# Performance work log

Measured on AMD Instinct MI355X. Metric: run time of the kernel, lower is better.

The kernel has to match this reference:

```python
import jax, jax.numpy as jnp
import numpy as np
from jax import lax

B, D, N, M = 512, 1024, 8192, 2048  # batch, input_dim, n_sdr, n_minicolumns
K = 4            # n_columns
W_SPARSE = 320   # SDR sparsity w (active bits per SDR)
K_ACTIVE = 40    # active minicolumns per step
PERM_THRESH = 0.5
LR = 0.01
CONSENSUS_THRESH = 1.0  # strict AND


def setup_inputs() -> dict:
    key = jax.random.key(0)
    k1, k2, k3 = jax.random.split(key, 3)
    s_batch = jax.random.normal(k1, (B, D), dtype=jnp.float32)
    W_enc = jax.random.normal(k2, (K, D, N), dtype=jnp.float32)  # per-column encoders (no weight sharing)
    perm = jax.random.uniform(k3, (K, M, N), dtype=jnp.float32)  # per-column permanences
    return {"s_batch": s_batch, "W_enc": W_enc, "perm": perm}


def _one_hot_topk(scores, k):
    # scores: [B, C] -> binary [B, C] with top-k per row set to 1
    _, idx = lax.top_k(scores, k)
    rows = jnp.arange(scores.shape[0])[:, None]
    return jnp.zeros_like(scores).at[rows, idx].set(1.0)


def reference(s_batch, W_enc, perm):
    def column(We, P):
        # SDRSpace.encode: random projection + top-w binarization
        scores = s_batch @ We                       # [B, N]
        sdr = _one_hot_topk(scores, W_SPARSE)       # [B, N] binary
        # SpatialPooler.forward_batch: overlap with connected synapses, top-k minicolumns
        connected = (P >= PERM_THRESH).astype(sdr.dtype)  # [M, N]
        overlap = sdr @ connected.T                 # [B, M]
        act = _one_hot_topk(overlap, K_ACTIVE)      # [B, M] binary winners
        # hebbian_update_batch: reinforce active inputs, punish inactive, on winning columns
        delta = (LR / B) * (act.T @ (2.0 * sdr - 1.0))    # [M, N] scatter-accumulated
        P_new = jnp.clip(P + delta, 0.0, 1.0)
        return sdr, P_new

    all_sdrs, perms_new = jax.vmap(column)(W_enc, perm)   # [K,B,N], [K,M,N]
    vote_fraction = all_sdrs.mean(axis=0)                  # [B, N]
    consensus = (vote_fraction >= CONSENSUS_THRESH).astype(jnp.float32)
    return consensus, all_sdrs[0], perms_new
```

## Files before the change

kernel.cpp:

```cpp
#include <hip/hip_runtime.h>
#include <stdint.h>

#define B_   512
#define D_   1024
#define N_   8192
#define M_   2048
#define K_   4
#define WSP  320
#define KACT 40
#define NW   128

typedef _Float16 f16;
typedef _Float16 f16x4 __attribute__((ext_vector_type(4)));
typedef _Float16 f16x8 __attribute__((ext_vector_type(8)));
typedef float f32x4 __attribute__((ext_vector_type(4)));

#define BM 128
#define BN 256
#define SPLIT_SCALE 2048.0f
#define SPLIT_INV (1.0f / 2048.0f)

#define GLD16(g, l) __builtin_amdgcn_global_load_lds( \
    (const __attribute__((address_space(1))) uint32_t*)(g), \
    (__attribute__((address_space(3))) uint32_t*)(l), 16, 0, 0)

__global__ __launch_bounds__(256) void prep_kernel(const float* __restrict__ perm,
                                                   uint32_t* __restrict__ conn32,
                                                   int* __restrict__ mcount,
                                                   const float* __restrict__ S,
                                                   uint8_t* __restrict__ imgA) {
    int bid = blockIdx.x;
    int tid = threadIdx.x;
    if (bid < 128) {
        int blk = bid;
        int mt = blk >> 5, dstep = blk & 31;
        uint8_t* outb = imgA + (size_t)blk * 16384;
#pragma unroll
        for (int q = 0; q < 4; q++) {
            int o = tid * 16 + q * 4096;
            int r = o >> 7, inner = o & 127;
            int sw = (r & 7) << 4;
            int raw = inner ^ sw;
            int plane = raw >> 6;
            int k0 = (raw & 63) >> 1;
            const float* sp = &S[(size_t)(mt * 128 + r) * D_ + dstep * 32 + k0];
            float4 v0 = *(const float4*)sp;
            float4 v1 = *(const float4*)(sp + 4);
            f16x8 out;
            if (plane == 0) {
                out[0] = (f16)v0.x; out[1] = (f16)v0.y; out[2] = (f16)v0.z; out[3] = (f16)v0.w;
                out[4] = (f16)v1.x; out[5] = (f16)v1.y; out[6] = (f16)v1.z; out[7] = (f16)v1.w;
            } else {
                f16 h0 = (f16)v0.x, h1 = (f16)v0.y, h2 = (f16)v0.z, h3 = (f16)v0.w;
                f16 h4 = (f16)v1.x, h5 = (f16)v1.y, h6 = (f16)v1.z, h7 = (f16)v1.w;
                out[0] = (f16)((v0.x - (float)h0) * SPLIT_SCALE);
                out[1] = (f16)((v0.y - (float)h1) * SPLIT_SCALE);
                out[2] = (f16)((v0.z - (float)h2) * SPLIT_SCALE);
                out[3] = (f16)((v0.w - (float)h3) * SPLIT_SCALE);
                out[4] = (f16)((v1.x - (float)h4) * SPLIT_SCALE);
                out[5] = (f16)((v1.y - (float)h5) * SPLIT_SCALE);
                out[6] = (f16)((v1.z - (float)h6) * SPLIT_SCALE);
                out[7] = (f16)((v1.w - (float)h7) * SPLIT_SCALE);
            }
            *(f16x8*)&outb[o] = out;
        }
        return;
    }
    int km = bid - 128;
    if (tid == 0) mcount[km] = 0;
    const float* p = perm + (size_t)km * N_ + tid * 32;
    uint32_t bits = 0;
#pragma unroll
    for (int q = 0; q < 8; q++) {
        float4 v = *(const float4*)&p[q * 4];
        bits |= (v.x >= 0.5f ? 1u : 0u) << (q * 4 + 0);
        bits |= (v.y >= 0.5f ? 1u : 0u) << (q * 4 + 1);
        bits |= (v.z >= 0.5f ? 1u : 0u) << (q * 4 + 2);
        bits |= (v.w >= 0.5f ? 1u : 0u) << (q * 4 + 3);
    }
    conn32[(size_t)km * 256 + tid] = bits;
}

__device__ __forceinline__ void pack_write_B(uint8_t* Bn, const float* w,
                                             int kc0, int bn, int bsw) {
#pragma unroll
    for (int kci = 0; kci < 2; kci++) {
        int kc = kc0 * 2 + kci;
        f16x8 hv, lv;
#pragma unroll
        for (int j = 0; j < 8; j++) {
            float x = w[kci * 8 + j];
            f16 h = (f16)x;
            hv[j] = h;
            lv[j] = (f16)((x - (float)h) * SPLIT_SCALE);
        }
        *(f16x8*)&Bn[bn * 128 + ((kc * 16) ^ bsw)] = hv;
        *(f16x8*)&Bn[bn * 128 + ((64 + kc * 16) ^ bsw)] = lv;
    }
}

__global__ __launch_bounds__(512, 2) void gemm_kernel(const uint8_t* __restrict__ imgA,
                                                      const float* __restrict__ W,
                                                      float* __restrict__ C) {
    __shared__ __align__(16) uint8_t lds[98304];

    int bid = blockIdx.x;
    int l = (bid & 7) * 64 + (bid >> 3);
    int mt = l & 3, nt = (l >> 2) & 31, kt = l >> 7;

    int tid = threadIdx.x;
    int wave = tid >> 6, lane = tid & 63;
    int wm = wave >> 2, wn = wave & 3;
    int lr = lane & 15, lg = lane >> 4;

    const uint8_t* srcA0 = imgA + (size_t)(mt * 32) * 16384 + wave * 1024 + lane * 16;

    const float* Wp = W + (size_t)kt * D_ * N_ + nt * BN;
    float* Cp = C + (size_t)kt * B_ * N_ + (size_t)(mt * BM) * N_ + nt * BN;

    int bn = tid & 255;
    int kc0 = tid >> 8;
    int bsw = (bn & 7) << 4;

    f32x4 acc0[4][4], acc1[4][4];
#pragma unroll
    for (int i = 0; i < 4; i++)
#pragma unroll
        for (int j = 0; j < 4; j++) {
            acc0[i][j] = (f32x4){0.f, 0.f, 0.f, 0.f};
            acc1[i][j] = (f32x4){0.f, 0.f, 0.f, 0.f};
        }

    {
        uint8_t* dA = lds + wave * 1024;
        GLD16(srcA0, dA);
        GLD16(srcA0 + 8192, dA + 8192);
        float w[16];
        const float* wp0 = Wp + (size_t)(kc0 * 16) * N_ + bn;
#pragma unroll
        for (int j = 0; j < 16; j++) w[j] = wp0[(size_t)j * N_];
        pack_write_B(lds + 32768, w, kc0, bn, bsw);
    }
    __syncthreads();

    for (int dstep = 0; dstep < 32; dstep++) {
        int cur = dstep & 1;
        uint8_t* Ac = lds + cur * 16384;
        uint8_t* Bc = lds + 32768 + cur * 32768;
        bool pf = (dstep < 31);

        float wreg[16];
        if (pf) {
            const uint8_t* sA = srcA0 + (size_t)(dstep + 1) * 16384;
            uint8_t* dA = lds + (cur ^ 1) * 16384 + wave * 1024;
            GLD16(sA, dA);
            GLD16(sA + 8192, dA + 8192);
            const float* wp0 = Wp + (size_t)((dstep + 1) * 32 + kc0 * 16) * N_ + bn;
#pragma unroll
            for (int j = 0; j < 16; j++) wreg[j] = wp0[(size_t)j * N_];
        }

        f16x8 ah[4], al[4];
#pragma unroll
        for (int i = 0; i < 4; i++) {
            int r = wm * 64 + i * 16 + lr;
            int sw = (r & 7) << 4;
            ah[i] = *(const f16x8*)&Ac[r * 128 + ((lg * 16) ^ sw)];
            al[i] = *(const f16x8*)&Ac[r * 128 + ((64 + lg * 16) ^ sw)];
        }
#pragma unroll
        for (int jj = 0; jj < 4; jj++) {
            int n = wn * 64 + jj * 16 + lr;
            int sw = (n & 7) << 4;
            f16x8 bh = *(const f16x8*)&Bc[n * 128 + ((lg * 16) ^ sw)];
            f16x8 bl = *(const f16x8*)&Bc[n * 128 + ((64 + lg * 16) ^ sw)];
            __builtin_amdgcn_s_setprio(1);
#pragma unroll
            for (int i = 0; i < 4; i++) {
                acc0[i][jj] = __builtin_amdgcn_mfma_f32_16x16x32_f16(ah[i], bh, acc0[i][jj], 0, 0, 0);
                acc1[i][jj] = __builtin_amdgcn_mfma_f32_16x16x32_f16(ah[i], bl, acc1[i][jj], 0, 0, 0);
                acc1[i][jj] = __builtin_amdgcn_mfma_f32_16x16x32_f16(al[i], bh, acc1[i][jj], 0, 0, 0);
            }
            __builtin_amdgcn_s_setprio(0);
        }

        if (pf)
            pack_write_B(lds + 32768 + (cur ^ 1) * 32768, wreg, kc0, bn, bsw);

        __syncthreads();
    }

#pragma unroll
    for (int i = 0; i < 4; i++)
#pragma unroll
        for (int jj = 0; jj < 4; jj++) {
            int r0 = wm * 64 + i * 16 + lg * 4;
            int c0 = wn * 64 + jj * 16 + lr;
#pragma unroll
            for (int r = 0; r < 4; r++)
                Cp[(size_t)(r0 + r) * N_ + c0] = acc0[i][jj][r] + acc1[i][jj][r] * SPLIT_INV;
        }
}

__global__ __launch_bounds__(256) void sdr_select_kernel(const float* __restrict__ scores,
                                                         uint32_t* __restrict__ sdr_bits32) {
    __shared__ int hist[256];
    __shared__ int scan2[256];
    __shared__ uint32_t sh_prefix;
    __shared__ int sh_r;

    int b = blockIdx.x;
    int k = blockIdx.y;
    int tid = threadIdx.x;
    const float* row = scores + ((size_t)k * B_ + b) * N_ + tid * 32;

    uint32_t key[32];
#pragma unroll
    for (int q = 0; q < 8; q++) {
        float4 v = *(const float4*)&row[q * 4];
        uint32_t u0 = __float_as_uint(v.x), u1 = __float_as_uint(v.y);
        uint32_t u2 = __float_as_uint(v.z), u3 = __float_as_uint(v.w);
        key[q * 4 + 0] = (u0 & 0x80000000u) ? ~u0 : (u0 | 0x80000000u);
        key[q * 4 + 1] = (u1 & 0x80000000u) ? ~u1 : (u1 | 0x80000000u);
        key[q * 4 + 2] = (u2 & 0x80000000u) ? ~u2 : (u2 | 0x80000000u);
        key[q * 4 + 3] = (u3 & 0x80000000u) ? ~u3 : (u3 | 0x80000000u);
    }
    if (tid == 0) { sh_prefix = 0u; sh_r = WSP; }
    __syncthreads();

    for (int p = 3; p >= 0; p--) {
        hist[tid] = 0;
        __syncthreads();
        uint32_t prefix = sh_prefix;
        int r = sh_r;
        uint32_t maskHi = (p == 3) ? 0u : (0xFFFFFFFFu << ((p + 1) * 8));
        int shift = p * 8;
#pragma unroll
        for (int j = 0; j < 32; j++) {
            uint32_t u = key[j];
            if ((u & maskHi) == prefix) atomicAdd(&hist[(u >> shift) & 255], 1);
        }
        __syncthreads();
#pragma unroll
        for (int off = 1; off < 256; off <<= 1) {
            int x = hist[tid] + ((tid + off < 256) ? hist[tid + off] : 0);
            __syncthreads();
            hist[tid] = x;
            __syncthreads();
        }
        int Sv = hist[tid];
        int Sn = (tid < 255) ? hist[tid + 1] : 0;
        if (Sv >= r && Sn < r) { sh_prefix = prefix | ((uint32_t)tid << shift); sh_r = r - Sn; }
        __syncthreads();
    }
    uint32_t t = sh_prefix;

    int gt = 0, eq = 0;
#pragma unroll
    for (int j = 0; j < 32; j++) {
        gt += (key[j] > t); eq += (key[j] == t);
    }
    hist[tid] = gt; scan2[tid] = eq;
    __syncthreads();
#pragma unroll
    for (int off = 1; off < 256; off <<= 1) {
        int g = hist[tid] + ((tid >= off) ? hist[tid - off] : 0);
        int e = scan2[tid] + ((tid >= off) ? scan2[tid - off] : 0);
        __syncthreads();
        hist[tid] = g; scan2[tid] = e;
        __syncthreads();
    }
    int totalGt = hist[255];
    int eb = scan2[tid] - eq;
    int r_eq = WSP - totalGt;

    uint32_t bits = 0;
#pragma unroll
    for (int j = 0; j < 32; j++) {
        uint32_t u = key[j];
        bool f = (u > t) || ((u == t) && (eb < r_eq));
        if (u == t) eb++;
        if (f) bits |= (1u << j);
    }
    sdr_bits32[((size_t)k * B_ + b) * 256 + tid] = bits;
}

#define OV_BBLK 16
#define OV_MTILE 512
__global__ __launch_bounds__(256) void overlap_mat_kernel(const uint64_t* __restrict__ sdr_bits,
                                                          const uint64_t* __restrict__ conn,
                                                          uint16_t* __restrict__ ovmat) {
    __shared__ uint64_t sw[OV_BBLK][NW];

    int bid = blockIdx.x;
    int nb = (bid & 7) * 64 + (bid >> 3);
    int k = nb >> 7;
    int rem = nb & 127;
    int b0 = (rem >> 2) * OV_BBLK;
    int m0 = (rem & 3) * OV_MTILE;
    int tid = threadIdx.x;

    for (int i = tid; i < OV_BBLK * NW; i += 256) {
        int bb = i >> 7, w = i & 127;
        sw[bb][w] = sdr_bits[((size_t)k * B_ + b0 + bb) * NW + w];
    }
    __syncthreads();

    int m_a = m0 + tid;
    int m_b = m0 + tid + 256;
    const ulonglong2* cra = (const ulonglong2*)(conn + ((size_t)k * M_ + m_a) * NW);
    const ulonglong2* crb = (const ulonglong2*)(conn + ((size_t)k * M_ + m_b) * NW);

    int acca[OV_BBLK], accb[OV_BBLK];
#pragma unroll
    for (int i = 0; i < OV_BBLK; i++) { acca[i] = 0; accb[i] = 0; }

#pragma unroll 2
    for (int wp = 0; wp < NW / 2; wp++) {
        ulonglong2 ca = cra[wp];
        ulonglong2 cb = crb[wp];
#pragma unroll
        for (int bb = 0; bb < OV_BBLK; bb++) {
            ulonglong2 s = *(const ulonglong2*)&sw[bb][wp * 2];
            acca[bb] += __popcll(ca.x & s.x) + __popcll(ca.y & s.y);
            accb[bb] += __popcll(cb.x & s.x) + __popcll(cb.y & s.y);
        }
    }
#pragma unroll
    for (int bb = 0; bb < OV_BBLK; bb++) {
        ovmat[((size_t)k * B_ + b0 + bb) * M_ + m_a] = (uint16_t)acca[bb];
        ovmat[((size_t)k * B_ + b0 + bb) * M_ + m_b] = (uint16_t)accb[bb];
    }
}

__global__ __launch_bounds__(256) void top40_kernel(const uint16_t* __restrict__ ovmat,
                                                    int* __restrict__ mcount,
                                                    int* __restrict__ mlist) {
    __shared__ int hist[512];
    __shared__ int scanbuf[256];
    __shared__ int sh_t, sh_req;

    int kb = blockIdx.x;
    int k = kb >> 9;
    int b = kb & 511;
    int tid = threadIdx.x;

    union { uint4 raw; uint16_t v[8]; } ov;
    ov.raw = *(const uint4*)&ovmat[(size_t)kb * M_ + tid * 8];

    hist[tid] = 0; hist[tid + 256] = 0;
    __syncthreads();
#pragma unroll
    for (int j = 0; j < 8; j++) atomicAdd(&hist[ov.v[j]], 1);
    __syncthreads();
#pragma unroll
    for (int off = 1; off < 512; off <<= 1) {
        int a0 = hist[tid] + ((tid + off < 512) ? hist[tid + off] : 0);
        int a1 = hist[tid + 256] + ((tid + 256 + off < 512) ? hist[tid + 256 + off] : 0);
        __syncthreads();
        hist[tid] = a0; hist[tid + 256] = a1;
        __syncthreads();
    }
#pragma unroll
    for (int which = 0; which < 2; which++) {
        int v = tid + which * 256;
        int Sv = hist[v];
        int Sn = (v < 511) ? hist[v + 1] : 0;
        if (Sv >= KACT && Sn < KACT) { sh_t = v; sh_req = KACT - Sn; }
    }
    __syncthreads();
    int t = sh_t, req = sh_req;
    int eq = 0;
#pragma unroll
    for (int j = 0; j < 8; j++) eq += (ov.v[j] == t);
    scanbuf[tid] = eq;
    __syncthreads();
#pragma unroll
    for (int off = 1; off < 256; off <<= 1) {
        int e = scanbuf[tid] + ((tid >= off) ? scanbuf[tid - off] : 0);
        __syncthreads();
        scanbuf[tid] = e;
        __syncthreads();
    }
    int eb = scanbuf[tid] - eq;
#pragma unroll
    for (int j = 0; j < 8; j++) {
        int m = tid * 8 + j;
        int v2 = ov.v[j];
        bool act = (v2 > t) || (v2 == t && eb < req);
        if (v2 == t) eb++;
        if (act) {
            int pos = atomicAdd(&mcount[k * M_ + m], 1);
            mlist[(((size_t)k * M_ + m) << 9) + pos] = b;
        }
    }
}

__global__ __launch_bounds__(512) void tail_kernel(const float* __restrict__ perm,
                                                   const uint64_t* __restrict__ sdr_bits,
                                                   const int* __restrict__ mcount,
                                                   const int* __restrict__ mlist,
                                                   float* __restrict__ pout,
                                                   float* __restrict__ cons,
                                                   float* __restrict__ sdr0) {
    __shared__ int blist[512];
    if (blockIdx.x >= 8192) {
        int gid = (blockIdx.x - 8192) * 512 + threadIdx.x;
        int b = gid >> 13;
        int n = gid & (N_ - 1);
        int wi = n >> 6, bit = n & 63;
        size_t base = (size_t)b * NW + wi;
        uint64_t w0 = sdr_bits[base];
        uint64_t w1 = sdr_bits[(size_t)1 * B_ * NW + base];
        uint64_t w2 = sdr_bits[(size_t)2 * B_ * NW + base];
        uint64_t w3 = sdr_bits[(size_t)3 * B_ * NW + base];
        uint64_t a = w0 & w1 & w2 & w3;
        cons[gid] = (float)((a >> bit) & 1);
        sdr0[gid] = (float)((w0 >> bit) & 1);
        return;
    }
    int km = blockIdx.x;
    int k = km / M_;
    int tid = threadIdx.x;
    int cnt = mcount[km];
    for (int i = tid; i < cnt; i += 512) blist[i] = mlist[((size_t)km << 9) + i];
    __syncthreads();

    int n0 = tid * 16;
    int c[16];
#pragma unroll
    for (int j = 0; j < 16; j++) c[j] = 0;
    int wi = n0 >> 6;
    int sh = n0 & 63;
    const uint64_t* sb = sdr_bits + (size_t)k * B_ * NW;
    for (int i = 0; i < cnt; i++) {
        uint64_t wv = sb[(size_t)blist[i] * NW + wi];
        unsigned bits = (unsigned)((wv >> sh) & 0xFFFFu);
#pragma unroll
        for (int j = 0; j < 16; j++) c[j] += (bits >> j) & 1;
    }
    const float scale = (float)(0.01 / 512.0);
    const float* pr = perm + (size_t)km * N_ + n0;
    float* po = pout + (size_t)km * N_ + n0;
#pragma unroll
    for (int q = 0; q < 4; q++) {
        float4 pv = *(const float4*)&pr[q * 4];
        float4 o;
        o.x = fminf(fmaxf(pv.x + scale * (float)(2 * c[q * 4 + 0] - cnt), 0.f), 1.f);
        o.y = fminf(fmaxf(pv.y + scale * (float)(2 * c[q * 4 + 1] - cnt), 0.f), 1.f);
        o.z = fminf(fmaxf(pv.z + scale * (float)(2 * c[q * 4 + 2] - cnt), 0.f), 1.f);
        o.w = fminf(fmaxf(pv.w + scale * (float)(2 * c[q * 4 + 3] - cnt), 0.f), 1.f);
        *(float4*)&po[q * 4] = o;
    }
}

extern "C" void kernel_launch(void* const* d_in, const int* in_sizes, int n_in,
                              void* d_out, int out_size, void* d_ws, size_t ws_size,
                              hipStream_t stream) {
    const float* s_batch = (const float*)d_in[0];
    const float* W_enc   = (const float*)d_in[1];
    const float* perm    = (const float*)d_in[2];

    float* out  = (float*)d_out;
    float* cons = out;
    float* sdr0 = out + (size_t)B_ * N_;
    float* pout = out + (size_t)2 * B_ * N_;

    char* ws = (char*)d_ws;
    float*    scores   = (float*)ws;
    uint16_t* ovmat    = (uint16_t*)ws;
    uint64_t* sdr_bits = (uint64_t*)(ws + ((size_t)64 << 20));
    uint64_t* conn     = (uint64_t*)(ws + ((size_t)66 << 20));
    int*      mcount   = (int*)(ws + ((size_t)74 << 20));
    int*      mlist    = (int*)(ws + ((size_t)75 << 20));
    uint8_t*  imgA     = (uint8_t*)(ws + ((size_t)92 << 20));

    prep_kernel<<<8192 + 128, 256, 0, stream>>>(perm, (uint32_t*)conn, mcount,
                                                s_batch, imgA);

    gemm_kernel<<<K_ * (B_ / BM) * (N_ / BN), 512, 0, stream>>>(imgA, W_enc, scores);

    dim3 gs(B_, K_);
    sdr_select_kernel<<<gs, 256, 0, stream>>>(scores, (uint32_t*)sdr_bits);

    overlap_mat_kernel<<<K_ * (B_ / OV_BBLK) * (M_ / OV_MTILE), 256, 0, stream>>>(
        sdr_bits, conn, ovmat);
    top40_kernel<<<K_ * B_, 256, 0, stream>>>(ovmat, mcount, mlist);

    tail_kernel<<<16384, 512, 0, stream>>>(perm, sdr_bits, mcount, mlist,
                                           pout, cons, sdr0);
}
```

Before: 450.5 us.

## Switch top-k selection kernels to one row per wavefront with shuffle scans

The SDR top-320 and overlap top-40 selection kernels now handle one row per 64-lane wavefront instead of one row per 256-thread block. Block-wide shared-memory scans with many __syncthreads are replaced by wave shuffles and ballots. The SDR radix select drops from four 8-bit passes to three 11/11/10-bit passes over a per-wave 2048-bin histogram. Rows are re-read from global memory on each pass instead of kept in registers, trading extra (likely cached) loads for fewer barriers and fewer passes.

```diff
diff --git a/kernel.cpp b/kernel.cpp
--- a/kernel.cpp
+++ b/kernel.cpp
@@ -23,6 +23,10 @@
 #define GLD16(g, l) __builtin_amdgcn_global_load_lds( \
     (const __attribute__((address_space(1))) uint32_t*)(g), \
     (__attribute__((address_space(3))) uint32_t*)(l), 16, 0, 0)
+
+__device__ __forceinline__ uint32_t fkey(uint32_t u) {
+    return u ^ ((uint32_t)((int32_t)u >> 31) | 0x80000000u);
+}
 
 __global__ __launch_bounds__(256) void prep_kernel(const float* __restrict__ perm,
                                                    uint32_t* __restrict__ conn32,
@@ -204,85 +208,111 @@
 
 __global__ __launch_bounds__(256) void sdr_select_kernel(const float* __restrict__ scores,
                                                          uint32_t* __restrict__ sdr_bits32) {
-    __shared__ int hist[256];
-    __shared__ int scan2[256];
-    __shared__ uint32_t sh_prefix;
-    __shared__ int sh_r;
-
-    int b = blockIdx.x;
-    int k = blockIdx.y;
+    __shared__ uint32_t hist4[4][2048];
     int tid = threadIdx.x;
-    const float* row = scores + ((size_t)k * B_ + b) * N_ + tid * 32;
-
-    uint32_t key[32];
-#pragma unroll
-    for (int q = 0; q < 8; q++) {
-        float4 v = *(const float4*)&row[q * 4];
-        uint32_t u0 = __float_as_uint(v.x), u1 = __float_as_uint(v.y);
-        uint32_t u2 = __float_as_uint(v.z), u3 = __float_as_uint(v.w);
-        key[q * 4 + 0] = (u0 & 0x80000000u) ? ~u0 : (u0 | 0x80000000u);
-        key[q * 4 + 1] = (u1 & 0x80000000u) ? ~u1 : (u1 | 0x80000000u);
-        key[q * 4 + 2] = (u2 & 0x80000000u) ? ~u2 : (u2 | 0x80000000u);
-        key[q * 4 + 3] = (u3 & 0x80000000u) ? ~u3 : (u3 | 0x80000000u);
-    }
-    if (tid == 0) { sh_prefix = 0u; sh_r = WSP; }
-    __syncthreads();
-
-    for (int p = 3; p >= 0; p--) {
-        hist[tid] = 0;
-        __syncthreads();
-        uint32_t prefix = sh_prefix;
-        int r = sh_r;
-        uint32_t maskHi = (p == 3) ? 0u : (0xFFFFFFFFu << ((p + 1) * 8));
-        int shift = p * 8;
-#pragma unroll
-        for (int j = 0; j < 32; j++) {
-            uint32_t u = key[j];
-            if ((u & maskHi) == prefix) atomicAdd(&hist[(u >> shift) & 255], 1);
-        }
-        __syncthreads();
-#pragma unroll
-        for (int off = 1; off < 256; off <<= 1) {
-            int x = hist[tid] + ((tid + off < 256) ? hist[tid + off] : 0);
-            __syncthreads();
-            hist[tid] = x;
-            __syncthreads();
-        }
-        int Sv = hist[tid];
-        int Sn = (tid < 255) ? hist[tid + 1] : 0;
-        if (Sv >= r && Sn < r) { sh_prefix = prefix | ((uint32_t)tid << shift); sh_r = r - Sn; }
-        __syncthreads();
-    }
-    uint32_t t = sh_prefix;
+    int w = tid >> 6, lane = tid & 63;
+    int r = blockIdx.x * 4 + w;
+    uint32_t* hist = hist4[w];
+    const float* rowp = scores + (size_t)r * N_ + lane * 128;
+
+    uint32_t prefix = 0;
+    int rem = WSP;
+
+    for (int p = 0; p < 3; p++) {
+        const int shift = (p == 0) ? 21 : (p == 1) ? 10 : 0;
+        const uint32_t dm = (p == 2) ? 1023u : 2047u;
+        const uint32_t hm = (p == 0) ? 0u : (p == 1) ? 0xFFE00000u : 0xFFFFFC00u;
+        uint4 z = {0u, 0u, 0u, 0u};
+#pragma unroll
+        for (int q = 0; q < 8; q++)
+            ((uint4*)hist)[q * 64 + lane] = z;
+#pragma unroll 8
+        for (int q = 0; q < 32; q++) {
+            float4 fv = *(const float4*)&rowp[q * 4];
+            uint32_t k0 = fkey(__float_as_uint(fv.x));
+            uint32_t k1 = fkey(__float_as_uint(fv.y));
+            uint32_t k2 = fkey(__float_as_uint(fv.z));
+            uint32_t k3 = fkey(__float_as_uint(fv.w));
+            if ((k0 & hm) == prefix) { uint32_t d = (k0 >> shift) & dm; atomicAdd(&hist[((d & 31u) << 6) + (d >> 5)], 1u); }
+            if ((k1 & hm) == prefix) { uint32_t d = (k1 >> shift) & dm; atomicAdd(&hist[((d & 31u) << 6) + (d >> 5)], 1u); }
+            if ((k2 & hm) == prefix) { uint32_t d = (k2 >> shift) & dm; atomicAdd(&hist[((d & 31u) << 6) + (d >> 5)], 1u); }
+            if ((k3 & hm) == prefix) { uint32_t d = (k3 >> shift) & dm; atomicAdd(&hist[((d & 31u) << 6) + (d >> 5)], 1u); }
+        }
+        asm volatile("s_waitcnt lgkmcnt(0)" ::: "memory");
+        uint32_t h[32];
+#pragma unroll
+        for (int i = 0; i < 32; i++) h[i] = hist[i * 64 + lane];
+        int L = 0;
+#pragma unroll
+        for (int i = 0; i < 32; i++) L += (int)h[i];
+        int S = L;
+#pragma unroll
+        for (int off = 1; off < 64; off <<= 1) {
+            int t2 = __shfl_down(S, off);
+            if (lane + off < 64) S += t2;
+        }
+        int Snext = __shfl_down(S, 1);
+        if (lane == 63) Snext = 0;
+        bool cross = (S >= rem) && (Snext < rem);
+        unsigned long long bal = __ballot(cross);
+        int cl = __ffsll((long long)bal) - 1;
+        int vd = 0, rp2 = 0, found = 0;
+        int acc = Snext;
+#pragma unroll
+        for (int i = 31; i >= 0; i--) {
+            int prev = acc;
+            acc += (int)h[i];
+            if (!found && acc >= rem) { vd = lane * 32 + i; rp2 = rem - prev; found = 1; }
+        }
+        int dig = __shfl(vd, cl);
+        rem = __shfl(rp2, cl);
+        prefix |= (uint32_t)dig << shift;
+    }
+    uint32_t t = prefix;
 
     int gt = 0, eq = 0;
-#pragma unroll
-    for (int j = 0; j < 32; j++) {
-        gt += (key[j] > t); eq += (key[j] == t);
-    }
-    hist[tid] = gt; scan2[tid] = eq;
-    __syncthreads();
-#pragma unroll
-    for (int off = 1; off < 256; off <<= 1) {
-        int g = hist[tid] + ((tid >= off) ? hist[tid - off] : 0);
-        int e = scan2[tid] + ((tid >= off) ? scan2[tid - off] : 0);
-        __syncthreads();
-        hist[tid] = g; scan2[tid] = e;
-        __syncthreads();
-    }
-    int totalGt = hist[255];
-    int eb = scan2[tid] - eq;
+#pragma unroll 8
+    for (int q = 0; q < 32; q++) {
+        float4 fv = *(const float4*)&rowp[q * 4];
+        uint32_t k0 = fkey(__float_as_uint(fv.x));
+        uint32_t k1 = fkey(__float_as_uint(fv.y));
+        uint32_t k2 = fkey(__float_as_uint(fv.z));
+        uint32_t k3 = fkey(__float_as_uint(fv.w));
+        gt += (k0 > t) + (k1 > t) + (k2 > t) + (k3 > t);
+        eq += (k0 == t) + (k1 == t) + (k2 == t) + (k3 == t);
+    }
+    int totalGt = gt;
+#pragma unroll
+    for (int off = 1; off < 64; off <<= 1) totalGt += __shfl_xor(totalGt, off);
+    int eqIncl = eq;
+#pragma unroll
+    for (int off = 1; off < 64; off <<= 1) {
+        int t3 = __shfl_up(eqIncl, off);
+        if (lane >= off) eqIncl += t3;
+    }
+    int eb = eqIncl - eq;
     int r_eq = WSP - totalGt;
 
-    uint32_t bits = 0;
-#pragma unroll
-    for (int j = 0; j < 32; j++) {
-        uint32_t u = key[j];
-        bool f = (u > t) || ((u == t) && (eb < r_eq));
-        if (u == t) eb++;
-        if (f) bits |= (1u << j);
-    }
-    sdr_bits32[((size_t)k * B_ + b) * 256 + tid] = bits;
+    uint32_t wd[4];
+#pragma unroll
+    for (int c = 0; c < 4; c++) wd[c] = 0u;
+#pragma unroll 8
+    for (int q = 0; q < 32; q++) {
+        float4 fv = *(const float4*)&rowp[q * 4];
+        uint32_t k0 = fkey(__float_as_uint(fv.x));
+        uint32_t k1 = fkey(__float_as_uint(fv.y));
+        uint32_t k2 = fkey(__float_as_uint(fv.z));
+        uint32_t k3 = fkey(__float_as_uint(fv.w));
+        bool f0 = (k0 > t) || ((k0 == t) && (eb < r_eq)); if (k0 == t) eb++;
+        bool f1 = (k1 > t) || ((k1 == t) && (eb < r_eq)); if (k1 == t) eb++;
+        bool f2 = (k2 > t) || ((k2 == t) && (eb < r_eq)); if (k2 == t) eb++;
+        bool f3 = (k3 > t) || ((k3 == t) && (eb < r_eq)); if (k3 == t) eb++;
+        int base = (q * 4) & 31;
+        wd[q >> 3] |= ((uint32_t)f0 << base) | ((uint32_t)f1 << (base + 1)) |
+                      ((uint32_t)f2 << (base + 2)) | ((uint32_t)f3 << (base + 3));
+    }
+    uint4 outv = {wd[0], wd[1], wd[2], wd[3]};
+    *(uint4*)&sdr_bits32[(size_t)r * 256 + lane * 4] = outv;
 }
 
 #define OV_BBLK 16
@@ -336,59 +366,78 @@
 __global__ __launch_bounds__(256) void top40_kernel(const uint16_t* __restrict__ ovmat,
                                                     int* __restrict__ mcount,
                                                     int* __restrict__ mlist) {
-    __shared__ int hist[512];
-    __shared__ int scanbuf[256];
-    __shared__ int sh_t, sh_req;
-
-    int kb = blockIdx.x;
-    int k = kb >> 9;
-    int b = kb & 511;
+    __shared__ uint32_t hist4[4][512];
     int tid = threadIdx.x;
-
-    union { uint4 raw; uint16_t v[8]; } ov;
-    ov.raw = *(const uint4*)&ovmat[(size_t)kb * M_ + tid * 8];
-
-    hist[tid] = 0; hist[tid + 256] = 0;
-    __syncthreads();
-#pragma unroll
-    for (int j = 0; j < 8; j++) atomicAdd(&hist[ov.v[j]], 1);
-    __syncthreads();
-#pragma unroll
-    for (int off = 1; off < 512; off <<= 1) {
-        int a0 = hist[tid] + ((tid + off < 512) ? hist[tid + off] : 0);
-        int a1 = hist[tid + 256] + ((tid + 256 + off < 512) ? hist[tid + 256 + off] : 0);
-        __syncthreads();
-        hist[tid] = a0; hist[tid + 256] = a1;
-        __syncthreads();
-    }
-#pragma unroll
-    for (int which = 0; which < 2; which++) {
-        int v = tid + which * 256;
-        int Sv = hist[v];
-        int Sn = (v < 511) ? hist[v + 1] : 0;
-        if (Sv >= KACT && Sn < KACT) { sh_t = v; sh_req = KACT - Sn; }
-    }
-    __syncthreads();
-    int t = sh_t, req = sh_req;
+    int w = tid >> 6, lane = tid & 63;
+    int r = blockIdx.x * 4 + w;
+    int k = r >> 9, b = r & 511;
+    uint32_t* hist = hist4[w];
+
+    const uint4* rp4 = (const uint4*)(ovmat + (size_t)r * M_ + lane * 32);
+    int v[32];
+#pragma unroll
+    for (int c = 0; c < 4; c++) {
+        uint4 raw = rp4[c];
+        v[c * 8 + 0] = raw.x & 0xFFFF; v[c * 8 + 1] = raw.x >> 16;
+        v[c * 8 + 2] = raw.y & 0xFFFF; v[c * 8 + 3] = raw.y >> 16;
+        v[c * 8 + 4] = raw.z & 0xFFFF; v[c * 8 + 5] = raw.z >> 16;
+        v[c * 8 + 6] = raw.w & 0xFFFF; v[c * 8 + 7] = raw.w >> 16;
+    }
+    uint4 z = {0u, 0u, 0u, 0u};
+    ((uint4*)hist)[lane] = z;
+    ((uint4*)hist)[64 + lane] = z;
+#pragma unroll
+    for (int j = 0; j < 32; j++) {
+        int d = v[j];
+        atomicAdd(&hist[((d & 31) << 4) + (d >> 5)], 1u);
+    }
+    asm volatile("s_waitcnt lgkmcnt(0)" ::: "memory");
+    uint32_t h[8];
+#pragma unroll
+    for (int i = 0; i < 8; i++) {
+        int bin = lane * 8 + i;
+        h[i] = hist[((bin & 31) << 4) + (bin >> 5)];
+    }
+    int L = 0;
+#pragma unroll
+    for (int i = 0; i < 8; i++) L += (int)h[i];
+    int S = L;
+#pragma unroll
+    for (int off = 1; off < 64; off <<= 1) {
+        int t2 = __shfl_down(S, off);
+        if (lane + off < 64) S += t2;
+    }
+    int Snext = __shfl_down(S, 1);
+    if (lane == 63) Snext = 0;
+    bool cross = (S >= KACT) && (Snext < KACT);
+    unsigned long long bal = __ballot(cross);
+    int cl = __ffsll((long long)bal) - 1;
+    int vd = 0, rq = 0, found = 0;
+    int acc = Snext;
+#pragma unroll
+    for (int i = 7; i >= 0; i--) {
+        int prev = acc;
+        acc += (int)h[i];
+        if (!found && acc >= KACT) { vd = lane * 8 + i; rq = KACT - prev; found = 1; }
+    }
+    int t = __shfl(vd, cl);
+    int req = __shfl(rq, cl);
+
     int eq = 0;
 #pragma unroll
-    for (int j = 0; j < 8; j++) eq += (ov.v[j] == t);
-    scanbuf[tid] = eq;
-    __syncthreads();
-#pragma unroll
-    for (int off = 1; off < 256; off <<= 1) {
-        int e = scanbuf[tid] + ((tid >= off) ? scanbuf[tid - off] : 0);
-        __syncthreads();
-        scanbuf[tid] = e;
-        __syncthreads();
-    }
-    int eb = scanbuf[tid] - eq;
-#pragma unroll
-    for (int j = 0; j < 8; j++) {
-        int m = tid * 8 + j;
-        int v2 = ov.v[j];
-        bool act = (v2 > t) || (v2 == t && eb < req);
-        if (v2 == t) eb++;
+    for (int j = 0; j < 32; j++) eq += (v[j] == t);
+    int eqIncl = eq;
+#pragma unroll
+    for (int off = 1; off < 64; off <<= 1) {
+        int t3 = __shfl_up(eqIncl, off);
+        if (lane >= off) eqIncl += t3;
+    }
+    int eb = eqIncl - eq;
+#pragma unroll
+    for (int j = 0; j < 32; j++) {
+        int m = lane * 32 + j;
+        bool act = (v[j] > t) || ((v[j] == t) && (eb < req));
+        if (v[j] == t) eb++;
         if (act) {
             int pos = atomicAdd(&mcount[k * M_ + m], 1);
             mlist[(((size_t)k * M_ + m) << 9) + pos] = b;
@@ -480,12 +529,12 @@
 
     gemm_kernel<<<K_ * (B_ / BM) * (N_ / BN), 512, 0, stream>>>(imgA, W_enc, scores);
 
-    dim3 gs(B_, K_);
-    sdr_select_kernel<<<gs, 256, 0, stream>>>(scores, (uint32_t*)sdr_bits);
+    sdr_select_kernel<<<K_ * B_ / 4, 256, 0, stream>>>(scores, (uint32_t*)sdr_bits);
 
     overlap_mat_kernel<<<K_ * (B_ / OV_BBLK) * (M_ / OV_MTILE), 256, 0, stream>>>(
         sdr_bits, conn, ovmat);
-    top40_kernel<<<K_ * B_, 256, 0, stream>>>(ovmat, mcount, mlist);
+
+    top40_kernel<<<K_ * B_ / 4, 256, 0, stream>>>(ovmat, mcount, mlist);
 
     tail_kernel<<<16384, 512, 0, stream>>>(perm, sdr_bits, mcount, mlist,
                                            pout, cons, sdr0);
```

Result: slower. 489.7 us (+8.7%).

## Rebalance kernel fusion: move conn prep into select, consensus into top40

Applied to the files above, without the earlier changes.

Splits the prep kernel so the S split-precision conversion runs alone before the GEMM. The permanence-to-bitmask conversion now runs as extra blocks of the SDR select kernel, and the consensus/sdr0 output writes run as extra blocks of the top-40 kernel. The aim is to shorten the work ahead of the GEMM and fill the light select and top-40 launches with independent work. The Hebbian update becomes its own kernel. Launch count stays the same, but heterogeneous blocks in one grid can cause imbalance.

```diff
diff --git a/kernel.cpp b/kernel.cpp
--- a/kernel.cpp
+++ b/kernel.cpp
@@ -24,61 +24,41 @@
     (const __attribute__((address_space(1))) uint32_t*)(g), \
     (__attribute__((address_space(3))) uint32_t*)(l), 16, 0, 0)
 
-__global__ __launch_bounds__(256) void prep_kernel(const float* __restrict__ perm,
-                                                   uint32_t* __restrict__ conn32,
-                                                   int* __restrict__ mcount,
-                                                   const float* __restrict__ S,
-                                                   uint8_t* __restrict__ imgA) {
-    int bid = blockIdx.x;
-    int tid = threadIdx.x;
-    if (bid < 128) {
-        int blk = bid;
-        int mt = blk >> 5, dstep = blk & 31;
-        uint8_t* outb = imgA + (size_t)blk * 16384;
-#pragma unroll
-        for (int q = 0; q < 4; q++) {
-            int o = tid * 16 + q * 4096;
-            int r = o >> 7, inner = o & 127;
-            int sw = (r & 7) << 4;
-            int raw = inner ^ sw;
-            int plane = raw >> 6;
-            int k0 = (raw & 63) >> 1;
-            const float* sp = &S[(size_t)(mt * 128 + r) * D_ + dstep * 32 + k0];
-            float4 v0 = *(const float4*)sp;
-            float4 v1 = *(const float4*)(sp + 4);
-            f16x8 out;
-            if (plane == 0) {
-                out[0] = (f16)v0.x; out[1] = (f16)v0.y; out[2] = (f16)v0.z; out[3] = (f16)v0.w;
-                out[4] = (f16)v1.x; out[5] = (f16)v1.y; out[6] = (f16)v1.z; out[7] = (f16)v1.w;
-            } else {
-                f16 h0 = (f16)v0.x, h1 = (f16)v0.y, h2 = (f16)v0.z, h3 = (f16)v0.w;
-                f16 h4 = (f16)v1.x, h5 = (f16)v1.y, h6 = (f16)v1.z, h7 = (f16)v1.w;
-                out[0] = (f16)((v0.x - (float)h0) * SPLIT_SCALE);
-                out[1] = (f16)((v0.y - (float)h1) * SPLIT_SCALE);
-                out[2] = (f16)((v0.z - (float)h2) * SPLIT_SCALE);
-                out[3] = (f16)((v0.w - (float)h3) * SPLIT_SCALE);
-                out[4] = (f16)((v1.x - (float)h4) * SPLIT_SCALE);
-                out[5] = (f16)((v1.y - (float)h5) * SPLIT_SCALE);
-                out[6] = (f16)((v1.z - (float)h6) * SPLIT_SCALE);
-                out[7] = (f16)((v1.w - (float)h7) * SPLIT_SCALE);
-            }
-            *(f16x8*)&outb[o] = out;
-        }
-        return;
-    }
-    int km = bid - 128;
-    if (tid == 0) mcount[km] = 0;
-    const float* p = perm + (size_t)km * N_ + tid * 32;
-    uint32_t bits = 0;
-#pragma unroll
-    for (int q = 0; q < 8; q++) {
-        float4 v = *(const float4*)&p[q * 4];
-        bits |= (v.x >= 0.5f ? 1u : 0u) << (q * 4 + 0);
-        bits |= (v.y >= 0.5f ? 1u : 0u) << (q * 4 + 1);
-        bits |= (v.z >= 0.5f ? 1u : 0u) << (q * 4 + 2);
-        bits |= (v.w >= 0.5f ? 1u : 0u) << (q * 4 + 3);
-    }
-    conn32[(size_t)km * 256 + tid] = bits;
+__global__ __launch_bounds__(256) void splitS_kernel(const float* __restrict__ S,
+                                                     uint8_t* __restrict__ imgA) {
+    int blk = blockIdx.x;
+    int mt = blk >> 5, dstep = blk & 31;
+    int tid = threadIdx.x;
+    uint8_t* outb = imgA + (size_t)blk * 16384;
+#pragma unroll
+    for (int q = 0; q < 4; q++) {
+        int o = tid * 16 + q * 4096;
+        int r = o >> 7, inner = o & 127;
+        int sw = (r & 7) << 4;
+        int raw = inner ^ sw;
+        int plane = raw >> 6;
+        int k0 = (raw & 63) >> 1;
+        const float* sp = &S[(size_t)(mt * 128 + r) * D_ + dstep * 32 + k0];
+        float4 v0 = *(const float4*)sp;
+        float4 v1 = *(const float4*)(sp + 4);
+        f16x8 out;
+        if (plane == 0) {
+            out[0] = (f16)v0.x; out[1] = (f16)v0.y; out[2] = (f16)v0.z; out[3] = (f16)v0.w;
+            out[4] = (f16)v1.x; out[5] = (f16)v1.y; out[6] = (f16)v1.z; out[7] = (f16)v1.w;
+        } else {
+            f16 h0 = (f16)v0.x, h1 = (f16)v0.y, h2 = (f16)v0.z, h3 = (f16)v0.w;
+            f16 h4 = (f16)v1.x, h5 = (f16)v1.y, h6 = (f16)v1.z, h7 = (f16)v1.w;
+            out[0] = (f16)((v0.x - (float)h0) * SPLIT_SCALE);
+            out[1] = (f16)((v0.y - (float)h1) * SPLIT_SCALE);
+            out[2] = (f16)((v0.z - (float)h2) * SPLIT_SCALE);
+            out[3] = (f16)((v0.w - (float)h3) * SPLIT_SCALE);
+            out[4] = (f16)((v1.x - (float)h4) * SPLIT_SCALE);
+            out[5] = (f16)((v1.y - (float)h5) * SPLIT_SCALE);
+            out[6] = (f16)((v1.z - (float)h6) * SPLIT_SCALE);
+            out[7] = (f16)((v1.w - (float)h7) * SPLIT_SCALE);
+        }
+        *(f16x8*)&outb[o] = out;
+    }
 }
 
 __device__ __forceinline__ void pack_write_B(uint8_t* Bn, const float* w,
@@ -202,17 +182,37 @@
         }
 }
 
-__global__ __launch_bounds__(256) void sdr_select_kernel(const float* __restrict__ scores,
-                                                         uint32_t* __restrict__ sdr_bits32) {
+__global__ __launch_bounds__(256) void select_conn_kernel(const float* __restrict__ scores,
+                                                          uint32_t* __restrict__ sdr_bits32,
+                                                          const float* __restrict__ perm,
+                                                          uint32_t* __restrict__ conn32,
+                                                          int* __restrict__ mcount) {
+    int bid = blockIdx.x;
+    int tid = threadIdx.x;
+    if (bid >= 2048) {
+        int km = bid - 2048;
+        if (tid == 0) mcount[km] = 0;
+        const float* p = perm + (size_t)km * N_ + tid * 32;
+        uint32_t bits = 0;
+#pragma unroll
+        for (int q = 0; q < 8; q++) {
+            float4 v = *(const float4*)&p[q * 4];
+            bits |= (v.x >= 0.5f ? 1u : 0u) << (q * 4 + 0);
+            bits |= (v.y >= 0.5f ? 1u : 0u) << (q * 4 + 1);
+            bits |= (v.z >= 0.5f ? 1u : 0u) << (q * 4 + 2);
+            bits |= (v.w >= 0.5f ? 1u : 0u) << (q * 4 + 3);
+        }
+        conn32[(size_t)km * 256 + tid] = bits;
+        return;
+    }
+
     __shared__ int hist[256];
     __shared__ int scan2[256];
     __shared__ uint32_t sh_prefix;
     __shared__ int sh_r;
 
-    int b = blockIdx.x;
-    int k = blockIdx.y;
-    int tid = threadIdx.x;
-    const float* row = scores + ((size_t)k * B_ + b) * N_ + tid * 32;
+    int kb = bid;
+    const float* row = scores + (size_t)kb * N_ + tid * 32;
 
     uint32_t key[32];
 #pragma unroll
@@ -282,7 +282,7 @@
         if (u == t) eb++;
         if (f) bits |= (1u << j);
     }
-    sdr_bits32[((size_t)k * B_ + b) * 256 + tid] = bits;
+    sdr_bits32[(size_t)kb * 256 + tid] = bits;
 }
 
 #define OV_BBLK 16
@@ -333,79 +333,16 @@
     }
 }
 
-__global__ __launch_bounds__(256) void top40_kernel(const uint16_t* __restrict__ ovmat,
-                                                    int* __restrict__ mcount,
-                                                    int* __restrict__ mlist) {
-    __shared__ int hist[512];
-    __shared__ int scanbuf[256];
-    __shared__ int sh_t, sh_req;
-
-    int kb = blockIdx.x;
-    int k = kb >> 9;
-    int b = kb & 511;
-    int tid = threadIdx.x;
-
-    union { uint4 raw; uint16_t v[8]; } ov;
-    ov.raw = *(const uint4*)&ovmat[(size_t)kb * M_ + tid * 8];
-
-    hist[tid] = 0; hist[tid + 256] = 0;
-    __syncthreads();
-#pragma unroll
-    for (int j = 0; j < 8; j++) atomicAdd(&hist[ov.v[j]], 1);
-    __syncthreads();
-#pragma unroll
-    for (int off = 1; off < 512; off <<= 1) {
-        int a0 = hist[tid] + ((tid + off < 512) ? hist[tid + off] : 0);
-        int a1 = hist[tid + 256] + ((tid + 256 + off < 512) ? hist[tid + 256 + off] : 0);
-        __syncthreads();
-        hist[tid] = a0; hist[tid + 256] = a1;
-        __syncthreads();
-    }
-#pragma unroll
-    for (int which = 0; which < 2; which++) {
-        int v = tid + which * 256;
-        int Sv = hist[v];
-        int Sn = (v < 511) ? hist[v + 1] : 0;
-        if (Sv >= KACT && Sn < KACT) { sh_t = v; sh_req = KACT - Sn; }
-    }
-    __syncthreads();
-    int t = sh_t, req = sh_req;
-    int eq = 0;
-#pragma unroll
-    for (int j = 0; j < 8; j++) eq += (ov.v[j] == t);
-    scanbuf[tid] = eq;
-    __syncthreads();
-#pragma unroll
-    for (int off = 1; off < 256; off <<= 1) {
-        int e = scanbuf[tid] + ((tid >= off) ? scanbuf[tid - off] : 0);
-        __syncthreads();
-        scanbuf[tid] = e;
-        __syncthreads();
-    }
-    int eb = scanbuf[tid] - eq;
-#pragma unroll
-    for (int j = 0; j < 8; j++) {
-        int m = tid * 8 + j;
-        int v2 = ov.v[j];
-        bool act = (v2 > t) || (v2 == t && eb < req);
-        if (v2 == t) eb++;
-        if (act) {
-            int pos = atomicAdd(&mcount[k * M_ + m], 1);
-            mlist[(((size_t)k * M_ + m) << 9) + pos] = b;
-        }
-    }
-}
-
-__global__ __launch_bounds__(512) void tail_kernel(const float* __restrict__ perm,
-                                                   const uint64_t* __restrict__ sdr_bits,
-                                                   const int* __restrict__ mcount,
-                                                   const int* __restrict__ mlist,
-                                                   float* __restrict__ pout,
-                                                   float* __restrict__ cons,
-                                                   float* __restrict__ sdr0) {
-    __shared__ int blist[512];
-    if (blockIdx.x >= 8192) {
-        int gid = (blockIdx.x - 8192) * 512 + threadIdx.x;
+__global__ __launch_bounds__(256) void top40_cons_kernel(const uint16_t* __restrict__ ovmat,
+                                                         int* __restrict__ mcount,
+                                                         int* __restrict__ mlist,
+                                                         const uint64_t* __restrict__ sdr_bits,
+                                                         float* __restrict__ cons,
+                                                         float* __restrict__ sdr0) {
+    int bid = blockIdx.x;
+    int tid = threadIdx.x;
+    if (bid >= 2048) {
+        int gid = (bid - 2048) * 256 + tid;
         int b = gid >> 13;
         int n = gid & (N_ - 1);
         int wi = n >> 6, bit = n & 63;
@@ -419,6 +356,72 @@
         sdr0[gid] = (float)((w0 >> bit) & 1);
         return;
     }
+
+    __shared__ int hist[512];
+    __shared__ int scanbuf[256];
+    __shared__ int sh_t, sh_req;
+
+    int kb = bid;
+    int k = kb >> 9;
+    int b = kb & 511;
+
+    union { uint4 raw; uint16_t v[8]; } ov;
+    ov.raw = *(const uint4*)&ovmat[(size_t)kb * M_ + tid * 8];
+
+    hist[tid] = 0; hist[tid + 256] = 0;
+    __syncthreads();
+#pragma unroll
+    for (int j = 0; j < 8; j++) atomicAdd(&hist[ov.v[j]], 1);
+    __syncthreads();
+#pragma unroll
+    for (int off = 1; off < 512; off <<= 1) {
+        int a0 = hist[tid] + ((tid + off < 512) ? hist[tid + off] : 0);
+        int a1 = hist[tid + 256] + ((tid + 256 + off < 512) ? hist[tid + 256 + off] : 0);
+        __syncthreads();
+        hist[tid] = a0; hist[tid + 256] = a1;
+        __syncthreads();
+    }
+#pragma unroll
+    for (int which = 0; which < 2; which++) {
+        int v = tid + which * 256;
+        int Sv = hist[v];
+        int Sn = (v < 511) ? hist[v + 1] : 0;
+        if (Sv >= KACT && Sn < KACT) { sh_t = v; sh_req = KACT - Sn; }
+    }
+    __syncthreads();
+    int t = sh_t, req = sh_req;
+    int eq = 0;
+#pragma unroll
+    for (int j = 0; j < 8; j++) eq += (ov.v[j] == t);
+    scanbuf[tid] = eq;
+    __syncthreads();
+#pragma unroll
+    for (int off = 1; off < 256; off <<= 1) {
+        int e = scanbuf[tid] + ((tid >= off) ? scanbuf[tid - off] : 0);
+        __syncthreads();
+        scanbuf[tid] = e;
+        __syncthreads();
+    }
+    int eb = scanbuf[tid] - eq;
+#pragma unroll
+    for (int j = 0; j < 8; j++) {
+        int m = tid * 8 + j;
+        int v2 = ov.v[j];
+        bool act = (v2 > t) || (v2 == t && eb < req);
+        if (v2 == t) eb++;
+        if (act) {
+            int pos = atomicAdd(&mcount[k * M_ + m], 1);
+            mlist[(((size_t)k * M_ + m) << 9) + pos] = b;
+        }
+    }
+}
+
+__global__ __launch_bounds__(512) void update_kernel(const float* __restrict__ perm,
+                                                     const uint64_t* __restrict__ sdr_bits,
+                                                     const int* __restrict__ mcount,
+                                                     const int* __restrict__ mlist,
+                                                     float* __restrict__ pout) {
+    __shared__ int blist[512];
     int km = blockIdx.x;
     int k = km / M_;
     int tid = threadIdx.x;
@@ -475,18 +478,18 @@
     int*      mlist    = (int*)(ws + ((size_t)75 << 20));
     uint8_t*  imgA     = (uint8_t*)(ws + ((size_t)92 << 20));
 
-    prep_kernel<<<8192 + 128, 256, 0, stream>>>(perm, (uint32_t*)conn, mcount,
-                                                s_batch, imgA);
+    splitS_kernel<<<4 * 32, 256, 0, stream>>>(s_batch, imgA);
 
     gemm_kernel<<<K_ * (B_ / BM) * (N_ / BN), 512, 0, stream>>>(imgA, W_enc, scores);
 
-    dim3 gs(B_, K_);
-    sdr_select_kernel<<<gs, 256, 0, stream>>>(scores, (uint32_t*)sdr_bits);
+    select_conn_kernel<<<2048 + K_ * M_, 256, 0, stream>>>(
+        scores, (uint32_t*)sdr_bits, perm, (uint32_t*)conn, mcount);
 
     overlap_mat_kernel<<<K_ * (B_ / OV_BBLK) * (M_ / OV_MTILE), 256, 0, stream>>>(
         sdr_bits, conn, ovmat);
-    top40_kernel<<<K_ * B_, 256, 0, stream>>>(ovmat, mcount, mlist);
-
-    tail_kernel<<<16384, 512, 0, stream>>>(perm, sdr_bits, mcount, mlist,
-                                           pout, cons, sdr0);
-}
+
+    top40_cons_kernel<<<2048 + (B_ * N_) / 256, 256, 0, stream>>>(
+        ovmat, mcount, mlist, sdr_bits, cons, sdr0);
+
+    update_kernel<<<K_ * M_, 512, 0, stream>>>(perm, sdr_bits, mcount, mlist, pout);
+}
```

After: 434.9 us. 1.04x faster.
